# Optimization experiments

Hardware: AMD Instinct MI355X
Metric: run time of the kernel (lower is better)

## Reference

```python
import jax, jax.numpy as jnp
import numpy as np

B, D, U = 64, 256, 256

def setup_inputs() -> dict:
    key = jax.random.key(0)
    ks = jax.random.split(key, 16)
    init_mu = 0.05
    inputs = jax.random.normal(ks[0], (B, D), jnp.float32)
    prev_state = 0.1 * jax.random.normal(ks[1], (B, U), jnp.float32)
    A = jax.random.normal(ks[2], (B, U, U), jnp.float32)
    # symmetric, diagonally boosted covariance-like state
    Sigma_state = 0.01 * (A + jnp.swapaxes(A, 1, 2)) + 0.1 * jnp.eye(U, dtype=jnp.float32)
    def w(k, shape):
        return init_mu * jax.random.normal(k, shape, jnp.float32)
    def s(k):
        return jax.random.uniform(k, (U,), jnp.float32, -4.5, -2.2)
    return {
        'inputs': inputs, 'prev_state': prev_state, 'Sigma_state': Sigma_state,
        'U_z': w(ks[3], (D, U)), 'uz_sigma': s(ks[4]), 'W_z': w(ks[5], (U, U)), 'wz_sigma': s(ks[6]),
        'U_r': w(ks[7], (D, U)), 'ur_sigma': s(ks[8]), 'W_r': w(ks[9], (U, U)), 'wr_sigma': s(ks[10]),
        'U_h': w(ks[11], (D, U)), 'uh_sigma': s(ks[12]), 'W_h': w(ks[13], (U, U)), 'wh_sigma': s(ks[14]),
    }

def _outer(a, b):  # [B,u],[B,u] -> [B,u,u]
    return a[:, :, None] * b[:, None, :]

def _quad(W, S):  # W^T @ S @ W, S is [B,u,u]
    return jnp.matmul(jnp.matmul(W.T, S), W)

def _x_sigma_w(x, sv):  # ||x||^2 * diag(softplus sigma)
    return jnp.sum(x * x, axis=1)[:, None, None] * jnp.diag(sv)

def _tr_sigma_w(S, sv):  # trace(S) * diag(softplus sigma)
    return jnp.trace(S, axis1=1, axis2=2)[:, None, None] * jnp.diag(sv)

def _hadamard_sigma(S1, S2, m1, m2):
    # S1*S2 + diag(m1) S2 diag(m1) + diag(m2) S1 diag(m2) as elementwise/broadcast
    return S1 * S2 + _outer(m1, m1) * S2 + _outer(m2, m2) * S1

def reference(inputs, prev_state, Sigma_state, U_z, uz_sigma, W_z, wz_sigma,
              U_r, ur_sigma, W_r, wr_sigma, U_h, uh_sigma, W_h, wh_sigma):
    sp = jax.nn.softplus
    # --- z gate ---
    az = inputs @ U_z + prev_state @ W_z
    z = jax.nn.sigmoid(az)
    gz = z * (1.0 - z)  # d sigmoid
    Sz = (_quad(W_z, Sigma_state) + _x_sigma_w(prev_state, sp(wz_sigma))
          + _tr_sigma_w(Sigma_state, sp(wz_sigma)) + _x_sigma_w(inputs, sp(uz_sigma)))
    Sigma_out_z = Sz * _outer(gz, gz)
    # --- r gate ---
    ar = inputs @ U_r + prev_state @ W_r
    r = jax.nn.sigmoid(ar)
    gr = r * (1.0 - r)
    Sr = (_quad(W_r, Sigma_state) + _x_sigma_w(prev_state, sp(wr_sigma))
          + _tr_sigma_w(Sigma_state, sp(wr_sigma)) + _x_sigma_w(inputs, sp(ur_sigma)))
    Sigma_out_r = Sr * _outer(gr, gr)
    # --- h candidate ---
    g_in = prev_state * r
    ah = inputs @ U_h + g_in @ W_h
    h = jnp.tanh(ah)
    gh = 1.0 - h * h  # d tanh
    sigma_g = _hadamard_sigma(Sigma_state, Sigma_out_r, prev_state, r)
    Sh = (_quad(W_h, sigma_g) + _x_sigma_w(g_in, sp(wh_sigma))
          + _tr_sigma_w(sigma_g, sp(wh_sigma)) + _x_sigma_w(inputs, sp(uh_sigma)))
    Sigma_out_h = Sh * _outer(gh, gh)
    # --- output combination ---
    mu_out = z * prev_state + (1.0 - z) * h
    sigma_a = _hadamard_sigma(Sigma_out_z, Sigma_state, z, prev_state)
    sigma_b = _hadamard_sigma(Sigma_out_z, Sigma_out_h, 1.0 - z, h)
    Sigma_out = (sigma_a + sigma_b
                 - Sigma_out_z * _outer(prev_state, h)
                 - Sigma_out_z * _outer(h, prev_state))
    Sigma_out = jnp.where(jnp.isnan(Sigma_out) | jnp.isinf(Sigma_out),
                          jnp.zeros_like(Sigma_out), Sigma_out)
    eye = jnp.eye(Sigma_out.shape[-1], dtype=Sigma_out.dtype)
    d = jnp.abs(jnp.diagonal(Sigma_out, axis1=1, axis2=2))
    Sigma_out = Sigma_out * (1.0 - eye) + d[:, :, None] * eye
    return mu_out, Sigma_out
```

## Files before the change

kernel.cpp:

```cpp
#include <hip/hip_runtime.h>
#include <math.h>

#define UDIM 256
#define BATCH 64
#define MATN 65536
#define PITCH 280
#define GG_BASE 256
#define TRG_BASE 1280

typedef __bf16 bf16x8 __attribute__((ext_vector_type(8)));
typedef float  f32x4  __attribute__((ext_vector_type(4)));

__device__ __forceinline__ float softplusf(float x) { return log1pf(expf(x)); }
__device__ __forceinline__ float sigmoidf_(float x) { return 1.f/(1.f+expf(-x)); }

__device__ __forceinline__ bf16x8 frag_load(const __bf16* base, int rt, int kt, int lane) {
  return *(const bf16x8*)(base + (((size_t)(rt*8 + kt))*64 + lane)*8);
}

__device__ __forceinline__ bf16x8 cvt8(const float* p) {
  const float4 f0 = *(const float4*)p;
  const float4 f1 = *(const float4*)(p + 4);
  bf16x8 v;
  v[0]=(__bf16)f0.x; v[1]=(__bf16)f0.y; v[2]=(__bf16)f0.z; v[3]=(__bf16)f0.w;
  v[4]=(__bf16)f1.x; v[5]=(__bf16)f1.y; v[6]=(__bf16)f1.z; v[7]=(__bf16)f1.w;
  return v;
}

#define MFMA16 __builtin_amdgcn_mfma_f32_16x16x32_bf16

__global__ __launch_bounds__(256) void prep_all(
    const float* __restrict__ Uz, const float* __restrict__ Wz,
    const float* __restrict__ Ur, const float* __restrict__ Wr,
    const float* __restrict__ Uh, const float* __restrict__ Wh,
    __bf16* __restrict__ Fw_z, __bf16* __restrict__ Fw_r,
    __bf16* __restrict__ Fu_h, __bf16* __restrict__ Fw_h,
    const float* __restrict__ S, const float* __restrict__ x,
    const float* __restrict__ prev, float* __restrict__ scal,
    __bf16* __restrict__ Sf,
    float* __restrict__ zb, float* __restrict__ rb,
    float* __restrict__ gzb, float* __restrict__ grb,
    float* __restrict__ gin)
{
  const int bid = blockIdx.x;
  const int t = threadIdx.x;
  const int w = t >> 6, l = t & 63, r = l & 15, q = l >> 4;

  __shared__ __align__(16) unsigned char LDSU[16896];

  if (bid < 64) {
    const int mat = bid >> 4, tl = bid & 15;
    const int n0 = (tl & 3)*64, k0 = (tl >> 2)*64;
    const float* W; __bf16* F;
    switch (mat) {
      case 0: W = Wz; F = Fw_z; break;  case 1: W = Wr; F = Fw_r; break;
      case 2: W = Uh; F = Fu_h; break;  default: W = Wh; F = Fw_h; break;
    }
    float (*tile)[65] = (float (*)[65])LDSU;
    const int tx = t & 15, ty = t >> 4;
#pragma unroll
    for (int rr = 0; rr < 4; ++rr) {
      const int row = ty*4 + rr;
      const float4 f = *(const float4*)(W + (size_t)(k0 + row)*UDIM + n0 + tx*4);
      tile[row][tx*4+0] = f.x; tile[row][tx*4+1] = f.y;
      tile[row][tx*4+2] = f.z; tile[row][tx*4+3] = f.w;
    }
    __syncthreads();
#pragma unroll
    for (int ss = 0; ss < 2; ++ss) {
      const int s = t + ss*256;
      const int rt_l = s >> 7, kt_l = (s >> 6) & 1, lane = s & 63;
      const int nl = rt_l*16 + (lane & 15), kb = kt_l*32 + (lane >> 4)*8;
      __align__(16) __bf16 tmp[8];
#pragma unroll
      for (int e = 0; e < 8; ++e) tmp[e] = (__bf16)tile[kb + e][nl];
      *(uint4*)(F + (((size_t)((((n0 >> 4) + rt_l)*8) + (k0 >> 5) + kt_l))*64 + lane)*8)
          = *(const uint4*)tmp;
    }
  } else if (bid < 80) {
    const int blk = bid - 64;
    const int b0 = blk*4 + (t >> 6);
    const float4 xv = *(const float4*)(x + b0*UDIM + l*4);
    float s0 = xv.x*xv.x + xv.y*xv.y + xv.z*xv.z + xv.w*xv.w;
    const float4 pv = *(const float4*)(prev + b0*UDIM + l*4);
    float s1 = pv.x*pv.x + pv.y*pv.y + pv.z*pv.z + pv.w*pv.w;
    float s2 = 0.f;
#pragma unroll
    for (int e = 0; e < 4; ++e)
      s2 += S[(size_t)b0*MATN + (size_t)(l*4 + e)*257];
    for (int off = 32; off; off >>= 1) {
      s0 += __shfl_down(s0, off);
      s1 += __shfl_down(s1, off);
      s2 += __shfl_down(s2, off);
    }
    if (l == 0) { scal[b0] = s0; scal[64 + b0] = s1; scal[128 + b0] = s2; }
  } else if (bid < 112) {
    const int u2 = bid - 80;
    const int g = u2 >> 4, un = u2 & 15;
    const int n0 = un * 16;
    const float* Um = g ? Ur : Uz;
    const float* Wm = g ? Wr : Wz;
    __bf16 (*Ut)[16][264] = (__bf16 (*)[16][264])LDSU;
    {
      float uv[16], wv[16];
      const float* ur_ = Um + (size_t)t*UDIM + n0;
      const float* wr_ = Wm + (size_t)t*UDIM + n0;
#pragma unroll
      for (int p4 = 0; p4 < 4; ++p4) {
        *(float4*)&uv[p4*4] = *(const float4*)(ur_ + p4*4);
        *(float4*)&wv[p4*4] = *(const float4*)(wr_ + p4*4);
      }
#pragma unroll
      for (int e = 0; e < 16; ++e) {
        Ut[0][e][t] = (__bf16)uv[e];
        Ut[1][e][t] = (__bf16)wv[e];
      }
    }
    __syncthreads();

    const int mrow = w*16 + r;
    f32x4 acc = {};
#pragma unroll
    for (int ks = 0; ks < 16; ++ks) {
      const int k0 = ks*32;
      const float* asrc;
      int src, koff;
      if (k0 < 256) { asrc = x    + (size_t)mrow*UDIM + k0         + q*8; src = 0; koff = k0; }
      else          { asrc = prev + (size_t)mrow*UDIM + (k0 - 256) + q*8; src = 1; koff = k0 - 256; }
      const bf16x8 af = cvt8(asrc);
      const bf16x8 bv = *(const bf16x8*)&Ut[src][r][koff + q*8];
      acc = MFMA16(af, bv, acc, 0, 0, 0);
    }
    const int n = n0 + r;
    if (g == 0) {
#pragma unroll
      for (int v = 0; v < 4; ++v) {
        const int m = w*16 + q*4 + v;
        const float zv = sigmoidf_(acc[v]);
        zb[m*UDIM + n]  = zv;
        gzb[m*UDIM + n] = zv * (1.f - zv);
      }
    } else {
      float ggp[4];
#pragma unroll
      for (int v = 0; v < 4; ++v) {
        const int m = w*16 + q*4 + v;
        const float rv = sigmoidf_(acc[v]);
        const float pv = prev[m*UDIM + n];
        const float g2 = pv * rv;
        rb[m*UDIM + n]  = rv;
        grb[m*UDIM + n] = rv * (1.f - rv);
        gin[m*UDIM + n] = g2;
        ggp[v] = g2 * g2;
      }
#pragma unroll
      for (int s2 = 1; s2 < 16; s2 <<= 1)
#pragma unroll
        for (int v = 0; v < 4; ++v) ggp[v] += __shfl_xor(ggp[v], s2);
      if (r == 0)
#pragma unroll
        for (int v = 0; v < 4; ++v)
          scal[GG_BASE + (w*16 + q*4 + v)*16 + un] = ggp[v];
    }
  }

  {
    const int c = bid;
    const int bx = c & 3, by = (c >> 2) & 3, b = c >> 4;
    const size_t sb = (size_t)b * MATN;
#pragma unroll
    for (int ss = 0; ss < 2; ++ss) {
      const int s = t + ss*256;
      const int chunk = s >> 6, lane = s & 63;
      const int rt_l = chunk >> 1, kt_l = chunk & 1;
      const int row = by*64 + rt_l*16 + (lane & 15);
      const int col = bx*64 + kt_l*32 + (lane >> 4)*8;
      const bf16x8 v = cvt8(S + sb + (size_t)row*UDIM + col);
      *(bf16x8*)(Sf + sb + (((size_t)((by*4 + rt_l)*8 + bx*2 + kt_l))*64 + lane)*8) = v;
    }
  }
}

__global__ __launch_bounds__(256, 4) void quad_zr_gh(
    const float* __restrict__ S, const __bf16* __restrict__ Sf,
    const float* __restrict__ prev,
    const float* __restrict__ rb, const float* __restrict__ gzb,
    const float* __restrict__ grb,
    const float* __restrict__ wz_s, const float* __restrict__ uz_s,
    const float* __restrict__ wr_s, const float* __restrict__ ur_s,
    const __bf16* __restrict__ Fw_z, const __bf16* __restrict__ Fw_r,
    float* __restrict__ scal, __bf16* __restrict__ Szb, __bf16* __restrict__ G,
    const float* __restrict__ x, const float* __restrict__ gin,
    const float* __restrict__ zb,
    const __bf16* __restrict__ Fu_h, const __bf16* __restrict__ Fw_h,
    float* __restrict__ hb, float* __restrict__ ghb, float* __restrict__ mu_out)
{
  const int bid = blockIdx.x;
  const int t = threadIdx.x, w = t >> 6, l = t & 63, r = l & 15, q = l >> 4;
  const int s = bid >> 6, b = bid & 63;

  __shared__ __align__(16) __bf16 T[2*16*PITCH];
  __shared__ float red4[4];
  __bf16* Tz = T;
  __bf16* Tr = T + 16*PITCH;

  if (bid >= 1020) {
    const int jt = bid - 1020;
    const int mrow = w*16 + r;
    f32x4 acc[4] = {};
#pragma unroll
    for (int ks = 0; ks < 16; ++ks) {
      const int k0 = ks*32;
      const float* asrc; const __bf16* B; int kk;
      if (k0 < 256) { asrc = x   + (size_t)mrow*UDIM + k0         + q*8; B = Fu_h; kk = k0; }
      else          { asrc = gin + (size_t)mrow*UDIM + (k0 - 256) + q*8; B = Fw_h; kk = k0 - 256; }
      const bf16x8 af = cvt8(asrc);
#pragma unroll
      for (int ni = 0; ni < 4; ++ni) {
        const bf16x8 bv = frag_load(B, jt*4 + ni, kk >> 5, l);
        acc[ni] = MFMA16(af, bv, acc[ni], 0, 0, 0);
      }
    }
#pragma unroll
    for (int ni = 0; ni < 4; ++ni) {
      const int n = jt*64 + ni*16 + r;
#pragma unroll
      for (int v = 0; v < 4; ++v) {
        const int m = w*16 + q*4 + v;
        const float hv = tanhf(acc[ni][v]);
        const float zv = zb[m*UDIM + n];
        hb[m*UDIM + n]  = hv;
        ghb[m*UDIM + n] = 1.f - hv*hv;
        mu_out[m*UDIM + n] = zv * prev[m*UDIM + n] + (1.f - zv) * hv;
      }
    }
  }

  const size_t sb = (size_t)b * MATN;
  const __bf16* Sfb = Sf + sb;

  f32x4 az[4] = {}, ar[4] = {};
#pragma unroll
  for (int kp = 0; kp < 4; ++kp) {
    bf16x8 wzf[2], wrf[2], sv[2][4];
#pragma unroll
    for (int u = 0; u < 2; ++u) {
      const int kt = kp*2 + u;
      wzf[u] = frag_load(Fw_z, s, kt, l);
      wrf[u] = frag_load(Fw_r, s, kt, l);
#pragma unroll
      for (int ct = 0; ct < 4; ++ct) sv[u][ct] = frag_load(Sfb, w*4 + ct, kt, l);
    }
#pragma unroll
    for (int u = 0; u < 2; ++u)
#pragma unroll
      for (int ct = 0; ct < 4; ++ct) {
        az[ct] = MFMA16(wzf[u], sv[u][ct], az[ct], 0, 0, 0);
        ar[ct] = MFMA16(wrf[u], sv[u][ct], ar[ct], 0, 0, 0);
      }
  }
#pragma unroll
  for (int ct = 0; ct < 4; ++ct)
#pragma unroll
    for (int v = 0; v < 4; ++v) {
      Tz[(q*4 + v)*PITCH + w*64 + ct*16 + r] = (__bf16)az[ct][v];
      Tr[(q*4 + v)*PITCH + w*64 + ct*16 + r] = (__bf16)ar[ct][v];
    }
  __syncthreads();

  const int ib = s*16 + q*4;
  const f32x4 gz4 = *(const f32x4*)(gzb + b*UDIM + ib);
  const f32x4 gr4 = *(const f32x4*)(grb + b*UDIM + ib);
  const f32x4 pp4 = *(const f32x4*)(prev + b*UDIM + ib);
  const f32x4 rr4 = *(const f32x4*)(rb + b*UDIM + ib);
  float Sv[16];
#pragma unroll
  for (int ct = 0; ct < 4; ++ct)
#pragma unroll
    for (int v = 0; v < 4; ++v)
      Sv[ct*4 + v] = S[sb + (size_t)(ib + v)*UDIM + (w*4 + ct)*16 + r];
  const float xx = scal[b];
  const float dscal = scal[64 + b] + scal[128 + b];

  f32x4 qz[4] = {}, qr[4] = {};
#pragma unroll
  for (int kt = 0; kt < 8; ++kt) {
    bf16x8 bwz[4], bwr[4];
#pragma unroll
    for (int ct = 0; ct < 4; ++ct) {
      bwz[ct] = frag_load(Fw_z, w*4 + ct, kt, l);
      bwr[ct] = frag_load(Fw_r, w*4 + ct, kt, l);
    }
    const bf16x8 atz = *(const bf16x8*)&Tz[r*PITCH + kt*32 + q*8];
    const bf16x8 atr = *(const bf16x8*)&Tr[r*PITCH + kt*32 + q*8];
#pragma unroll
    for (int ct = 0; ct < 4; ++ct) {
      qz[ct] = MFMA16(atz, bwz[ct], qz[ct], 0, 0, 0);
      qr[ct] = MFMA16(atr, bwr[ct], qr[ct], 0, 0, 0);
    }
  }

  {
    __align__(16) __bf16 o16[16];
#pragma unroll
    for (int ct = 0; ct < 4; ++ct) {
      const int j = (w*4 + ct)*16 + r;
      const float gj = gzb[b*UDIM + j];
#pragma unroll
      for (int v = 0; v < 4; ++v) {
        const int i = ib + v;
        float qv = qz[ct][v];
        if (i == j) qv += dscal*softplusf(wz_s[i]) + xx*softplusf(uz_s[i]);
        o16[ct*4 + v] = (__bf16)(qv * gz4[v] * gj);
      }
    }
    __bf16* dst = Szb + ((size_t)(b*16 + s)*256 + t)*16;
    *(uint4*)dst       = *(const uint4*)&o16[0];
    *(uint4*)(dst + 8) = *(const uint4*)&o16[8];
  }

  {
    float gvals[16];
    float trg = 0.f;
#pragma unroll
    for (int ct = 0; ct < 4; ++ct) {
      const int j = (w*4 + ct)*16 + r;
      const float gj = grb[b*UDIM + j];
      const float pj = prev[b*UDIM + j];
      const float rj = rb[b*UDIM + j];
#pragma unroll
      for (int v = 0; v < 4; ++v) {
        const int i = ib + v;
        float qv = qr[ct][v];
        if (i == j) qv += dscal*softplusf(wr_s[i]) + xx*softplusf(ur_s[i]);
        const float Sg = qv * gr4[v] * gj;
        const float sv = Sv[ct*4 + v];
        const float go = Sg*(sv + pp4[v]*pj) + rr4[v]*rj*sv;
        gvals[ct*4 + v] = go;
        if (i == j) trg += go;
      }
    }
    for (int off = 32; off; off >>= 1) trg += __shfl_down(trg, off);
    if (l == 0) red4[w] = trg;

    __syncthreads();
    if (t == 0)
      scal[TRG_BASE + b*16 + s] = red4[0] + red4[1] + red4[2] + red4[3];
#pragma unroll
    for (int ct = 0; ct < 4; ++ct)
#pragma unroll
      for (int v = 0; v < 4; ++v)
        Tr[(q*4 + v)*PITCH + w*64 + ct*16 + r] = (__bf16)gvals[ct*4 + v];
    __syncthreads();
#pragma unroll
    for (int ee = 0; ee < 2; ++ee) {
      const int e = t + ee*256;
      const int kt = e >> 6, le = e & 63;
      const uint4 vv = *(const uint4*)&Tr[(le & 15)*PITCH + kt*32 + (le >> 4)*8];
      *(uint4*)(G + sb + (((size_t)(s*8 + kt))*64 + le)*8) = vv;
    }
  }
}

__global__ __launch_bounds__(256, 4) void quad_h(
    const float* __restrict__ S, const __bf16* __restrict__ Szb,
    const float* __restrict__ prev, const float* __restrict__ zb,
    const float* __restrict__ hb, const float* __restrict__ ghb,
    const float* __restrict__ wh_s, const float* __restrict__ uh_s,
    const __bf16* __restrict__ Fw_h, const __bf16* __restrict__ G,
    const float* __restrict__ scal, float* __restrict__ out_sig)
{
  const int bid = blockIdx.x;
  const int s = bid >> 6, b = bid & 63;
  const size_t sb = (size_t)b * MATN;
  const int t = threadIdx.x, w = t >> 6, l = t & 63, r = l & 15, q = l >> 4;
  const __bf16* Gb = G + sb;

  __shared__ __align__(16) __bf16 Th[16*PITCH];

  f32x4 ah[4] = {};
#pragma unroll
  for (int kp = 0; kp < 4; ++kp) {
    bf16x8 af[2], bv[2][4];
#pragma unroll
    for (int u = 0; u < 2; ++u) {
      const int kt = kp*2 + u;
      af[u] = frag_load(Fw_h, s, kt, l);
#pragma unroll
      for (int ct = 0; ct < 4; ++ct) bv[u][ct] = frag_load(Gb, w*4 + ct, kt, l);
    }
#pragma unroll
    for (int u = 0; u < 2; ++u)
#pragma unroll
      for (int ct = 0; ct < 4; ++ct)
        ah[ct] = MFMA16(af[u], bv[u][ct], ah[ct], 0, 0, 0);
  }
#pragma unroll
  for (int ct = 0; ct < 4; ++ct)
#pragma unroll
    for (int v = 0; v < 4; ++v)
      Th[(q*4 + v)*PITCH + w*64 + ct*16 + r] = (__bf16)ah[ct][v];
  __syncthreads();

  const int ib = s*16 + q*4;
  const __bf16* szp = Szb + ((size_t)(b*16 + s)*256 + t)*16;
  __align__(16) __bf16 sz16[16];
  *(uint4*)&sz16[0] = *(const uint4*)szp;
  *(uint4*)&sz16[8] = *(const uint4*)(szp + 8);
  const f32x4 g4 = *(const f32x4*)(ghb + b*UDIM + ib);
  const f32x4 p4 = *(const f32x4*)(prev + b*UDIM + ib);
  const f32x4 z4 = *(const f32x4*)(zb + b*UDIM + ib);
  const f32x4 h4 = *(const f32x4*)(hb + b*UDIM + ib);
  float Sv[16], gjv[4], pjv[4], zjv[4], hjv[4];
#pragma unroll
  for (int ct = 0; ct < 4; ++ct) {
    const int j = (w*4 + ct)*16 + r;
    gjv[ct] = ghb[b*UDIM + j];
    pjv[ct] = prev[b*UDIM + j];
    zjv[ct] = zb[b*UDIM + j];
    hjv[ct] = hb[b*UDIM + j];
#pragma unroll
    for (int v = 0; v < 4; ++v)
      Sv[ct*4 + v] = S[sb + (size_t)(ib + v)*UDIM + j];
  }
  const float xx = scal[b];
  float dscal = 0.f;
#pragma unroll
  for (int e = 0; e < 4; ++e) {
    const f32x4 a = *(const f32x4*)(scal + GG_BASE + b*16 + e*4);
    const f32x4 c = *(const f32x4*)(scal + TRG_BASE + b*16 + e*4);
    dscal += a[0]+a[1]+a[2]+a[3] + c[0]+c[1]+c[2]+c[3];
  }

  f32x4 qh[4] = {};
#pragma unroll
  for (int kt = 0; kt < 8; ++kt) {
    bf16x8 bw[4];
#pragma unroll
    for (int ct = 0; ct < 4; ++ct) bw[ct] = frag_load(Fw_h, w*4 + ct, kt, l);
    const bf16x8 at = *(const bf16x8*)&Th[r*PITCH + kt*32 + q*8];
#pragma unroll
    for (int ct = 0; ct < 4; ++ct)
      qh[ct] = MFMA16(at, bw[ct], qh[ct], 0, 0, 0);
  }

#pragma unroll
  for (int ct = 0; ct < 4; ++ct) {
    const int j = (w*4 + ct)*16 + r;
#pragma unroll
    for (int v = 0; v < 4; ++v) {
      const int i = ib + v;
      float qv = qh[ct][v];
      if (i == j) qv += dscal*softplusf(wh_s[i]) + xx*softplusf(uh_s[i]);
      const float Sg = qv * g4[v] * gjv[ct];
      const float sv = Sv[ct*4 + v];
      const float sz = (float)sz16[ct*4 + v];
      float val = sv*(sz + z4[v]*zjv[ct])
                + sz*(p4[v] - h4[v])*(pjv[ct] - hjv[ct])
                + Sg*(sz + (1.f - z4[v])*(1.f - zjv[ct]));
      if (!isfinite(val)) val = 0.f;
      if (i == j) val = fabsf(val);
      out_sig[sb + (size_t)i*UDIM + j] = val;
    }
  }
}

extern "C" void kernel_launch(void* const* d_in, const int* in_sizes, int n_in,
                              void* d_out, int out_size, void* d_ws, size_t ws_size,
                              hipStream_t stream) {
  const float* x    = (const float*)d_in[0];
  const float* prev = (const float*)d_in[1];
  const float* S    = (const float*)d_in[2];
  const float* Uz   = (const float*)d_in[3];
  const float* uz_s = (const float*)d_in[4];
  const float* Wz   = (const float*)d_in[5];
  const float* wz_s = (const float*)d_in[6];
  const float* Ur   = (const float*)d_in[7];
  const float* ur_s = (const float*)d_in[8];
  const float* Wr   = (const float*)d_in[9];
  const float* wr_s = (const float*)d_in[10];
  const float* Uh   = (const float*)d_in[11];
  const float* uh_s = (const float*)d_in[12];
  const float* Wh   = (const float*)d_in[13];
  const float* wh_s = (const float*)d_in[14];

  float* out_mu  = (float*)d_out;
  float* out_sig = out_mu + BATCH*UDIM;

  float* ws   = (float*)d_ws;
  float* zb   = ws;
  float* rb   = zb  + BATCH*UDIM;
  float* gzb  = rb  + BATCH*UDIM;
  float* grb  = gzb + BATCH*UDIM;
  float* gin  = grb + BATCH*UDIM;
  float* hb   = gin + BATCH*UDIM;
  float* ghb  = hb  + BATCH*UDIM;
  float* scal = ghb + BATCH*UDIM;
  __bf16* bws  = (__bf16*)(scal + 2304);
  __bf16* Fw_z = bws;
  __bf16* Fw_r = Fw_z + MATN;
  __bf16* Fu_h = Fw_r + MATN;
  __bf16* Fw_h = Fu_h + MATN;
  const size_t BIG = (size_t)BATCH * MATN;
  __bf16* Szb = Fw_h + MATN;
  __bf16* G   = Szb + BIG;
  __bf16* Sf  = G + BIG;

  prep_all<<<dim3(1024), 256, 0, stream>>>(Uz, Wz, Ur, Wr, Uh, Wh,
      Fw_z, Fw_r, Fu_h, Fw_h, S, x, prev, scal, Sf,
      zb, rb, gzb, grb, gin);
  quad_zr_gh<<<dim3(1024), 256, 0, stream>>>(S, Sf, prev, rb, gzb, grb,
      wz_s, uz_s, wr_s, ur_s, Fw_z, Fw_r, scal, Szb, G,
      x, gin, zb, Fu_h, Fw_h, hb, ghb, out_mu);
  quad_h<<<dim3(1024), 256, 0, stream>>>(S, Szb, prev, zb, hb, ghb,
      wh_s, uh_s, Fw_h, G, scal, out_sig);
}
```

Baseline: 162.6 us.

## Spread h-candidate GEMM over 16 leading blocks and hoist per-column vector loads

The extra tanh/mu_out GEMM work moves from the last four blocks (each computing 64 columns) to the first sixteen blocks (each computing 16 columns), with K-loop loads batched four at a time. Spreading the tail work over more blocks, and running it early rather than at the end of the grid, is meant to shorten the straggler tail. The per-column gz/gr/prev/r values are now loaded once, up front next to the S loads, instead of inside each epilogue loop, so their latency overlaps the MFMA phase. The cost is that sixteen blocks now carry an uneven amount of extra work, and the hoisted values need more registers.

```diff
diff --git a/kernel.cpp b/kernel.cpp
--- a/kernel.cpp
+++ b/kernel.cpp
@@ -204,35 +204,36 @@
   __bf16* Tz = T;
   __bf16* Tr = T + 16*PITCH;
 
-  if (bid >= 1020) {
-    const int jt = bid - 1020;
+  if (bid < 16) {
+    const int un = bid;
     const int mrow = w*16 + r;
-    f32x4 acc[4] = {};
-#pragma unroll
-    for (int ks = 0; ks < 16; ++ks) {
-      const int k0 = ks*32;
-      const float* asrc; const __bf16* B; int kk;
-      if (k0 < 256) { asrc = x   + (size_t)mrow*UDIM + k0         + q*8; B = Fu_h; kk = k0; }
-      else          { asrc = gin + (size_t)mrow*UDIM + (k0 - 256) + q*8; B = Fw_h; kk = k0 - 256; }
-      const bf16x8 af = cvt8(asrc);
-#pragma unroll
-      for (int ni = 0; ni < 4; ++ni) {
-        const bf16x8 bv = frag_load(B, jt*4 + ni, kk >> 5, l);
-        acc[ni] = MFMA16(af, bv, acc[ni], 0, 0, 0);
-      }
-    }
-#pragma unroll
-    for (int ni = 0; ni < 4; ++ni) {
-      const int n = jt*64 + ni*16 + r;
-#pragma unroll
-      for (int v = 0; v < 4; ++v) {
-        const int m = w*16 + q*4 + v;
-        const float hv = tanhf(acc[ni][v]);
-        const float zv = zb[m*UDIM + n];
-        hb[m*UDIM + n]  = hv;
-        ghb[m*UDIM + n] = 1.f - hv*hv;
-        mu_out[m*UDIM + n] = zv * prev[m*UDIM + n] + (1.f - zv) * hv;
-      }
+    f32x4 acc = {};
+#pragma unroll
+    for (int kq = 0; kq < 4; ++kq) {
+      bf16x8 af[4], bv[4];
+#pragma unroll
+      for (int u = 0; u < 4; ++u) {
+        const int k0 = (kq*4 + u)*32;
+        if (k0 < 256) {
+          af[u] = cvt8(x   + (size_t)mrow*UDIM + k0 + q*8);
+          bv[u] = frag_load(Fu_h, un, k0 >> 5, l);
+        } else {
+          af[u] = cvt8(gin + (size_t)mrow*UDIM + (k0 - 256) + q*8);
+          bv[u] = frag_load(Fw_h, un, (k0 - 256) >> 5, l);
+        }
+      }
+#pragma unroll
+      for (int u = 0; u < 4; ++u) acc = MFMA16(af[u], bv[u], acc, 0, 0, 0);
+    }
+    const int n = un*16 + r;
+#pragma unroll
+    for (int v = 0; v < 4; ++v) {
+      const int m = w*16 + q*4 + v;
+      const float hv = tanhf(acc[v]);
+      const float zv = zb[m*UDIM + n];
+      hb[m*UDIM + n]  = hv;
+      ghb[m*UDIM + n] = 1.f - hv*hv;
+      mu_out[m*UDIM + n] = zv * prev[m*UDIM + n] + (1.f - zv) * hv;
     }
   }
 
@@ -273,12 +274,18 @@
   const f32x4 gr4 = *(const f32x4*)(grb + b*UDIM + ib);
   const f32x4 pp4 = *(const f32x4*)(prev + b*UDIM + ib);
   const f32x4 rr4 = *(const f32x4*)(rb + b*UDIM + ib);
-  float Sv[16];
-#pragma unroll
-  for (int ct = 0; ct < 4; ++ct)
+  float Sv[16], gjz[4], gjr[4], pjv[4], rjv[4];
+#pragma unroll
+  for (int ct = 0; ct < 4; ++ct) {
+    const int j = (w*4 + ct)*16 + r;
+    gjz[ct] = gzb[b*UDIM + j];
+    gjr[ct] = grb[b*UDIM + j];
+    pjv[ct] = prev[b*UDIM + j];
+    rjv[ct] = rb[b*UDIM + j];
 #pragma unroll
     for (int v = 0; v < 4; ++v)
-      Sv[ct*4 + v] = S[sb + (size_t)(ib + v)*UDIM + (w*4 + ct)*16 + r];
+      Sv[ct*4 + v] = S[sb + (size_t)(ib + v)*UDIM + j];
+  }
   const float xx = scal[b];
   const float dscal = scal[64 + b] + scal[128 + b];
 
@@ -305,13 +312,12 @@
 #pragma unroll
     for (int ct = 0; ct < 4; ++ct) {
       const int j = (w*4 + ct)*16 + r;
-      const float gj = gzb[b*UDIM + j];
 #pragma unroll
       for (int v = 0; v < 4; ++v) {
         const int i = ib + v;
         float qv = qz[ct][v];
         if (i == j) qv += dscal*softplusf(wz_s[i]) + xx*softplusf(uz_s[i]);
-        o16[ct*4 + v] = (__bf16)(qv * gz4[v] * gj);
+        o16[ct*4 + v] = (__bf16)(qv * gz4[v] * gjz[ct]);
       }
     }
     __bf16* dst = Szb + ((size_t)(b*16 + s)*256 + t)*16;
@@ -325,17 +331,14 @@
 #pragma unroll
     for (int ct = 0; ct < 4; ++ct) {
       const int j = (w*4 + ct)*16 + r;
-      const float gj = grb[b*UDIM + j];
-      const float pj = prev[b*UDIM + j];
-      const float rj = rb[b*UDIM + j];
 #pragma unroll
       for (int v = 0; v < 4; ++v) {
         const int i = ib + v;
         float qv = qr[ct][v];
         if (i == j) qv += dscal*softplusf(wr_s[i]) + xx*softplusf(ur_s[i]);
-        const float Sg = qv * gr4[v] * gj;
+        const float Sg = qv * gr4[v] * gjr[ct];
         const float sv = Sv[ct*4 + v];
-        const float go = Sg*(sv + pp4[v]*pj) + rr4[v]*rj*sv;
+        const float go = Sg*(sv + pp4[v]*pjv[ct]) + rr4[v]*rjv[ct]*sv;
         gvals[ct*4 + v] = go;
         if (i == j) trg += go;
       }
```

Result: faster. 152.0 us (median of 2 runs) (-6.5%).
